# Optimization experiments

Measured on AMD Instinct MI355X. Metric: run time of the kernel, lower is better.

## Reference

```python
import jax, jax.numpy as jnp
import numpy as np

N_NODES = 50000
N_EDGES = 800000
D_IN = 128
D_OUT = 128
NEG_SLOPE = 0.2


def setup_inputs() -> dict:
    key = jax.random.key(0)
    ks = jax.random.split(key, 6)
    stdv = 1.0 / np.sqrt(D_OUT)
    X = jax.random.normal(ks[0], (N_NODES, D_IN), dtype=jnp.float32)
    W = jax.random.uniform(ks[1], (D_IN, D_OUT), dtype=jnp.float32, minval=-stdv, maxval=stdv)
    W_r = jax.random.uniform(ks[2], (D_IN, D_OUT), dtype=jnp.float32, minval=-stdv, maxval=stdv)
    W_l = jax.random.uniform(ks[3], (D_IN, D_OUT), dtype=jnp.float32, minval=-stdv, maxval=stdv)
    src = jax.random.randint(ks[4], (N_EDGES,), 0, N_NODES, dtype=jnp.int32)
    dst = jax.random.randint(ks[5], (N_EDGES,), 0, N_NODES, dtype=jnp.int32)
    return {"X": X, "W": W, "W_r": W_r, "W_l": W_l, "src": src, "dst": dst}


def reference(X, W, W_r, W_l, src, dst):
    # Dense transforms (comb/agg feature paths)
    comb = X @ W            # [N, D_out]
    h_r = X @ W_r           # [N, D_out]
    h_l = X @ W_l           # [N, D_out]
    # SDDMM: per-edge score e_ij = dot(h_l[i], h_r[j]) at nonzeros of A
    e = jnp.sum(h_l[src] * h_r[dst], axis=-1)          # [E]
    e = jax.nn.leaky_relu(e, negative_slope=NEG_SLOPE)  # LeakyReLU(0.2) on edge values
    # SpMM aggregation: agg[i] = sum_{j in N(i)} e_ij * comb[j]
    msgs = e[:, None] * comb[dst]                       # [E, D_out]
    agg = jax.ops.segment_sum(msgs, src, num_segments=N_NODES)  # [N, D_out]
    return agg
```

## Files before the change

kernel.cpp:

```cpp
#include <hip/hip_runtime.h>
#include <hip/hip_bf16.h>

#define N_NODES 50000
#define N_EDGES 800000
#define D 128
#define NEG_SLOPE 0.2f
#define APAD 136

#define FB 196
#define BCAP 8192
#define CHUNK 2048
#define BIN_NBLK ((N_EDGES + CHUNK - 1) / CHUNK)
#define GROWS 64
#define GGRID ((N_NODES + GROWS - 1) / GROWS)
#define GEMM_LDS (D * APAD * 2 + GROWS * APAD * 2)

#define SPMM_NODES 8
#define SPMM_GRID (N_NODES / SPMM_NODES)
#define SPMM_LDS (D * APAD * 2 + 16 * APAD * 2 + 16 * 132 * 4)

typedef __attribute__((ext_vector_type(8))) short bf16x8;
typedef __attribute__((ext_vector_type(4))) float f32x4;

__device__ inline unsigned short f2bf(float f) {
    union { float f; unsigned u; } v; v.f = f;
    const unsigned r = v.u + 0x7FFF + ((v.u >> 16) & 1);
    return (unsigned short)(r >> 16);
}
__device__ inline unsigned fbits(float f) { union { float f; unsigned u; } v; v.f = f; return v.u; }
__device__ inline float ffrom(unsigned u) { union { unsigned u; float f; } v; v.u = u; return v.f; }

__device__ inline void unpack8(const float4 raw, float* o) {
    const unsigned w0 = fbits(raw.x), w1 = fbits(raw.y), w2 = fbits(raw.z), w3 = fbits(raw.w);
    o[0] = ffrom(w0 << 16); o[1] = ffrom(w0 & 0xffff0000u);
    o[2] = ffrom(w1 << 16); o[3] = ffrom(w1 & 0xffff0000u);
    o[4] = ffrom(w2 << 16); o[5] = ffrom(w2 & 0xffff0000u);
    o[6] = ffrom(w3 << 16); o[7] = ffrom(w3 & 0xffff0000u);
}

__device__ __forceinline__ float rsum16(float t) {
    union { float f; int i; } u, s;
    u.f = t;
    s.i = __builtin_amdgcn_update_dpp(0, u.i, 0x128, 0xF, 0xF, true); u.f += s.f;
    s.i = __builtin_amdgcn_update_dpp(0, u.i, 0x124, 0xF, 0xF, true); u.f += s.f;
    s.i = __builtin_amdgcn_update_dpp(0, u.i, 0x4E,  0xF, 0xF, true); u.f += s.f;
    s.i = __builtin_amdgcn_update_dpp(0, u.i, 0x39,  0xF, 0xF, true); u.f += s.f;
    return u.f;
}

__device__ __forceinline__ int scan256_incl_fast(int* wsum, int t, int v) {
    const int lane = t & 63;
    int x = v;
#pragma unroll
    for (int off = 1; off < 64; off <<= 1) {
        const int u = __shfl_up(x, off, 64);
        if (lane >= off) x += u;
    }
    if (lane == 63) wsum[t >> 6] = x;
    __syncthreads();
    int base = 0;
#pragma unroll
    for (int wv = 0; wv < 3; ++wv)
        base += (wv < (t >> 6)) ? wsum[wv] : 0;
    return x + base;
}

__device__ __forceinline__ int scan_incl_512(int* wsum, int t, int v) {
    const int lane = t & 63;
    int x = v;
#pragma unroll
    for (int off = 1; off < 64; off <<= 1) {
        const int u = __shfl_up(x, off, 64);
        if (lane >= off) x += u;
    }
    if (lane == 63) wsum[t >> 6] = x;
    __syncthreads();
    int base = 0;
#pragma unroll
    for (int wv = 0; wv < 7; ++wv)
        base += (wv < (t >> 6)) ? wsum[wv] : 0;
    return x + base;
}

__device__ __forceinline__ void stage_B_lds(unsigned short* Bs, const ushort* __restrict__ BT) {
    const int tid = threadIdx.x;
#pragma unroll
    for (int i = 0; i < 8; ++i) {
        const int idx = tid + i * 256;
        const int row = idx >> 4;
        const int c8 = (idx & 15) << 3;
        const float4 v = ((const float4*)BT)[idx];
        *(float4*)&Bs[row * APAD + c8] = v;
    }
}

template <bool OUT_F32>
__device__ __forceinline__ void mfma_from_lds(const unsigned short* Bs,
                                              const unsigned short* As,
                                              int rb, float* __restrict__ Cf,
                                              ushort* __restrict__ Cb, int nrows) {
    const int tid = threadIdx.x;
    const int w = tid >> 6, lane = tid & 63, m = lane & 15, kq = lane >> 4;
    f32x4 acc[8] = {};
    const unsigned short* Arow = &As[(w * 16 + m) * APAD + kq * 8];
#pragma unroll
    for (int kc = 0; kc < 4; ++kc) {
        const bf16x8 af = *(const bf16x8*)(Arow + kc * 32);
#pragma unroll
        for (int t2 = 0; t2 < 8; ++t2) {
            const bf16x8 bf = *(const bf16x8*)&Bs[(t2 * 16 + m) * APAD + kc * 32 + kq * 8];
            acc[t2] = __builtin_amdgcn_mfma_f32_16x16x32_bf16(af, bf, acc[t2], 0, 0, 0);
        }
    }
    const int orow0 = rb + w * 16 + kq * 4;
#pragma unroll
    for (int t2 = 0; t2 < 8; ++t2) {
#pragma unroll
        for (int r = 0; r < 4; ++r) {
            const int row = orow0 + r;
            if (row < nrows) {
                const size_t o = (size_t)row * D + t2 * 16 + m;
                if (OUT_F32) Cf[o] = acc[t2][r];
                else         Cb[o] = f2bf(acc[t2][r]);
            }
        }
    }
}

__global__ __launch_bounds__(256) void prep_kernel(const float* __restrict__ W_l,
                                                   const float* __restrict__ W_r,
                                                   const float* __restrict__ W,
                                                   ushort* __restrict__ MbT,
                                                   ushort* __restrict__ WbT,
                                                   int* __restrict__ bucket_fill) {
    if (blockIdx.x == 0) bucket_fill[threadIdx.x] = 0;
    const int a = blockIdx.x * 2 + (threadIdx.x >> 7);
    const int b2 = threadIdx.x & 127;
    float acc = 0.f;
#pragma unroll
    for (int c = 0; c < D; c += 4) {
        const float4 wl = *(const float4*)(W_l + a * D + c);
        const float4 wr = *(const float4*)(W_r + b2 * D + c);
        acc += wl.x * wr.x + wl.y * wr.y + wl.z * wr.z + wl.w * wr.w;
    }
    MbT[b2 * D + a] = f2bf(acc);
    WbT[b2 * D + a] = f2bf(W[a * D + b2]);
}

__global__ __launch_bounds__(256) void k1_kernel(const int* __restrict__ src,
                                                 const int* __restrict__ dst,
                                                 int* __restrict__ bucket_fill,
                                                 int2* __restrict__ binned,
                                                 const ushort* __restrict__ MbT,
                                                 const float4* __restrict__ Xf4,
                                                 ushort* __restrict__ Xb,
                                                 ushort* __restrict__ hMb) {
    __shared__ __align__(16) char smem[GEMM_LDS];
    const int bx = blockIdx.x;
    const int t = threadIdx.x;

    if (bx < BIN_NBLK) {
        int*  hist     = (int*)smem;
        int*  bstart   = hist + 256;
        int*  reserveS = bstart + 256;
        int*  fillL    = reserveS + 256;
        int2* pairs    = (int2*)(fillL + 256);
        int*  targ     = (int*)(pairs + CHUNK);
        const int e0 = bx * CHUNK;

        hist[t] = 0;
        __syncthreads();

        int s[8], d[8], b[8];
#pragma unroll
        for (int i = 0; i < 8; ++i) {
            const int e = e0 + i * 256 + t;
            if (e < N_EDGES) {
                s[i] = src[e]; d[i] = dst[e]; b[i] = s[i] >> 8;
                atomicAdd(&hist[b[i]], 1);
            } else b[i] = -1;
        }
        __syncthreads();
        const int hv = hist[t];
        const int incl = scan256_incl_fast(bstart, t, hv);
        const int mystart = incl - hv;
        reserveS[t] = hv ? atomicAdd(&bucket_fill[t], hv) : 0;
        __syncthreads();
        bstart[t] = mystart;
        fillL[t] = mystart;
        __syncthreads();
#pragma unroll
        for (int i = 0; i < 8; ++i) {
            if (b[i] >= 0) {
                const int p = atomicAdd(&fillL[b[i]], 1);
                pairs[p] = make_int2(s[i], d[i]);
                const int pos = reserveS[b[i]] + (p - bstart[b[i]]);
                targ[p] = (pos < BCAP) ? (b[i] * BCAP + pos) : -1;
            }
        }
        __syncthreads();
        const int nval = min(CHUNK, N_EDGES - e0);
        for (int j = t; j < nval; j += 256)
            if (targ[j] >= 0) binned[targ[j]] = pairs[j];
    } else {
        unsigned short* Bs = (unsigned short*)smem;
        unsigned short* As = Bs + D * APAD;
        const int rb = (bx - BIN_NBLK) * GROWS;

        stage_B_lds(Bs, MbT);
#pragma unroll
        for (int i = 0; i < 4; ++i) {
            const int f2 = t + i * 256;
            const int row = f2 >> 4;
            const int c8 = (f2 & 15) << 3;
            ushort4 lo = {0, 0, 0, 0}, hi = {0, 0, 0, 0};
            if (rb + row < N_NODES) {
                const float4 a = Xf4[(size_t)(rb + row) * 32 + (c8 >> 2)];
                const float4 b = Xf4[(size_t)(rb + row) * 32 + (c8 >> 2) + 1];
                lo.x = f2bf(a.x); lo.y = f2bf(a.y); lo.z = f2bf(a.z); lo.w = f2bf(a.w);
                hi.x = f2bf(b.x); hi.y = f2bf(b.y); hi.z = f2bf(b.z); hi.w = f2bf(b.w);
                ushort* gp = Xb + (size_t)(rb + row) * D + c8;
                *(ushort4*)gp = lo;
                *(ushort4*)(gp + 4) = hi;
            }
            *(ushort4*)&As[row * APAD + c8] = lo;
            *(ushort4*)&As[row * APAD + c8 + 4] = hi;
        }
        __syncthreads();
        mfma_from_lds<false>(Bs, As, rb, nullptr, hMb, N_NODES);
    }
}

__global__ __launch_bounds__(512) void fine_kernel(const int2* __restrict__ binned,
                                                   const int* __restrict__ bucket_fill,
                                                   int* __restrict__ offsets,
                                                   int* __restrict__ sorted_dst) {
    __shared__ int cntS[256];
    __shared__ int nh[256];
    __shared__ int fill[256];
    __shared__ int wsum[8];
    __shared__ int dstbuf[BCAP];
    const int b = blockIdx.x;
    const int t = threadIdx.x;

    int cv = 0;
    if (t < 256) cv = (t < FB) ? bucket_fill[t] : 0;
    const int incl = scan_incl_512(wsum, t, cv);
    if (t < 256) cntS[t] = incl;
    __syncthreads();
    const int base = (b == 0) ? 0 : cntS[b - 1];
    int cnt = cntS[b] - base;
    if (cnt > BCAP) cnt = BCAP;

    if (t < 256) nh[t] = 0;
    __syncthreads();
    const int2* bb = binned + (size_t)b * BCAP;
    for (int e = t; e < cnt; e += 512) atomicAdd(&nh[bb[e].x & 255], 1);
    __syncthreads();
    const int v = (t < 256) ? nh[t] : 0;
    const int incl2 = scan_incl_512(wsum, t, v);
    if (t < 256) {
        const int mystart = incl2 - v;
        const int node = b * 256 + t;
        if (node < N_NODES) offsets[node] = base + mystart;
        fill[t] = mystart;
    }
    __syncthreads();
    for (int e = t; e < cnt; e += 512) {
        const int2 sd = bb[e];
        const int p = atomicAdd(&fill[sd.x & 255], 1);
        dstbuf[p] = sd.y;
    }
    __syncthreads();
    for (int j = t; j < cnt; j += 512)
        sorted_dst[base + j] = dstbuf[j];
}

__global__ __launch_bounds__(1024, 8) void spmm_fused_kernel(const ushort* __restrict__ hMb,
                                                             const ushort* __restrict__ Xb,
                                                             const int* __restrict__ offsets,
                                                             const int* __restrict__ sorted_dst,
                                                             const ushort* __restrict__ WbT,
                                                             float* __restrict__ agg) {
    __shared__ __align__(16) char smem[SPMM_LDS];
    unsigned short* Ws = (unsigned short*)smem;
    unsigned short* As = Ws + D * APAD;
    float*          Pf = (float*)(As + 16 * APAD);
    const int tid = threadIdx.x;

#pragma unroll
    for (int i = 0; i < 2; ++i) {
        const int idx = tid + i * 1024;
        const int row = idx >> 4;
        const int c8 = (idx & 15) << 3;
        const float4 v = ((const float4*)WbT)[idx];
        *(float4*)&Ws[row * APAD + c8] = v;
    }
    if (tid < 272) ((ushort4*)(As + 8 * APAD))[tid] = make_ushort4(0, 0, 0, 0);

    const int wave = tid >> 6;
    const int lane = tid & 63;
    const int h = wave & 1;
    const int nl = wave >> 1;
    const int node = blockIdx.x * SPMM_NODES + nl;
    const int q = lane >> 4;
    const int ql = lane & 15;

    float hm[8];
    unpack8(*(const float4*)(hMb + (size_t)node * D + ql * 8), hm);

    const int start = offsets[node];
    const int end = (node == N_NODES - 1) ? N_EDGES : offsets[node + 1];

    float acc[8] = {0.f, 0.f, 0.f, 0.f, 0.f, 0.f, 0.f, 0.f};

    int idx = start + h * 4 + q;
    while (idx + 8 < end) {
        const int d0 = sorted_dst[idx];
        const int d1 = sorted_dst[idx + 8];
        const float4 r0 = *(const float4*)(Xb + (size_t)d0 * D + ql * 8);
        const float4 r1 = *(const float4*)(Xb + (size_t)d1 * D + ql * 8);
        float t0 = 0.f, t1 = 0.f;
        {
            float x[8];
            unpack8(r0, x);
#pragma unroll
            for (int j = 0; j < 8; ++j) t0 = fmaf(hm[j], x[j], t0);
            unpack8(r1, x);
#pragma unroll
            for (int j = 0; j < 8; ++j) t1 = fmaf(hm[j], x[j], t1);
        }
        t0 = rsum16(t0);
        t1 = rsum16(t1);
        const float e0 = t0 > 0.f ? t0 : NEG_SLOPE * t0;
        const float e1 = t1 > 0.f ? t1 : NEG_SLOPE * t1;
        {
            float x[8];
            unpack8(r0, x);
#pragma unroll
            for (int j = 0; j < 8; ++j) acc[j] = fmaf(e0, x[j], acc[j]);
            unpack8(r1, x);
#pragma unroll
            for (int j = 0; j < 8; ++j) acc[j] = fmaf(e1, x[j], acc[j]);
        }
        idx += 16;
    }
    if (idx < end) {
        const int d0 = sorted_dst[idx];
        const float4 r0 = *(const float4*)(Xb + (size_t)d0 * D + ql * 8);
        float t0 = 0.f;
        {
            float x[8];
            unpack8(r0, x);
#pragma unroll
            for (int j = 0; j < 8; ++j) t0 = fmaf(hm[j], x[j], t0);
        }
        t0 = rsum16(t0);
        const float e0 = t0 > 0.f ? t0 : NEG_SLOPE * t0;
        {
            float x[8];
            unpack8(r0, x);
#pragma unroll
            for (int j = 0; j < 8; ++j) acc[j] = fmaf(e0, x[j], acc[j]);
        }
    }

#pragma unroll
    for (int j = 0; j < 8; ++j) {
        acc[j] += __shfl_xor(acc[j], 16);
        acc[j] += __shfl_xor(acc[j], 32);
    }
    if (q == 0) {
        float* p = Pf + (h * 8 + nl) * 132 + ql * 8;
#pragma unroll
        for (int j = 0; j < 8; ++j) p[j] = acc[j];
    }
    __syncthreads();

    if (h == 0 && q == 0) {
        const float* p0 = Pf + nl * 132 + ql * 8;
        const float* p1 = Pf + (8 + nl) * 132 + ql * 8;
        ushort4 o0, o1;
        o0.x = f2bf(p0[0] + p1[0]); o0.y = f2bf(p0[1] + p1[1]);
        o0.z = f2bf(p0[2] + p1[2]); o0.w = f2bf(p0[3] + p1[3]);
        o1.x = f2bf(p0[4] + p1[4]); o1.y = f2bf(p0[5] + p1[5]);
        o1.z = f2bf(p0[6] + p1[6]); o1.w = f2bf(p0[7] + p1[7]);
        *(ushort4*)&As[nl * APAD + ql * 8] = o0;
        *(ushort4*)&As[nl * APAD + ql * 8 + 4] = o1;
    }
    __syncthreads();

    if (wave < 4) {
        const int m = lane & 15, kq = lane >> 4;
        f32x4 oacc[2] = {};
        const unsigned short* Arow = &As[m * APAD + kq * 8];
#pragma unroll
        for (int kc = 0; kc < 4; ++kc) {
            const bf16x8 af = *(const bf16x8*)(Arow + kc * 32);
#pragma unroll
            for (int tt = 0; tt < 2; ++tt) {
                const int t2 = wave * 2 + tt;
                const bf16x8 bf = *(const bf16x8*)&Ws[(t2 * 16 + m) * APAD + kc * 32 + kq * 8];
                oacc[tt] = __builtin_amdgcn_mfma_f32_16x16x32_bf16(af, bf, oacc[tt], 0, 0, 0);
            }
        }
        if (kq < 2) {
            const int rbase = blockIdx.x * SPMM_NODES + kq * 4;
#pragma unroll
            for (int tt = 0; tt < 2; ++tt) {
                const int t2 = wave * 2 + tt;
#pragma unroll
                for (int r = 0; r < 4; ++r) {
                    agg[(size_t)(rbase + r) * D + t2 * 16 + m] = oacc[tt][r];
                }
            }
        }
    }
}

extern "C" void kernel_launch(void* const* d_in, const int* in_sizes, int n_in,
                              void* d_out, int out_size, void* d_ws, size_t ws_size,
                              hipStream_t stream) {
    const float* X   = (const float*)d_in[0];
    const float* W   = (const float*)d_in[1];
    const float* W_r = (const float*)d_in[2];
    const float* W_l = (const float*)d_in[3];
    const int* src   = (const int*)d_in[4];
    const int* dst   = (const int*)d_in[5];
    float* agg = (float*)d_out;

    ushort* Xb          = (ushort*)d_ws;
    ushort* hMb         = Xb + (size_t)N_NODES * D;
    ushort* MbT         = hMb + (size_t)N_NODES * D;
    ushort* WbT         = MbT + D * D;
    int*    offsets     = (int*)(WbT + D * D);
    int*    sorted_dst  = offsets + N_NODES;
    int*    bucket_fill = sorted_dst + N_EDGES;
    int2*   binned      = (int2*)(bucket_fill + 256);

    prep_kernel<<<64, 256, 0, stream>>>(W_l, W_r, W, MbT, WbT, bucket_fill);

    k1_kernel<<<BIN_NBLK + GGRID, 256, 0, stream>>>(
        src, dst, bucket_fill, binned, MbT, (const float4*)X, Xb, hMb);

    fine_kernel<<<FB, 512, 0, stream>>>(binned, bucket_fill, offsets, sorted_dst);

    spmm_fused_kernel<<<SPMM_GRID, 1024, 0, stream>>>(
        hMb, Xb, offsets, sorted_dst, WbT, agg);
}
```

Measured before the change: 167.7 us.

## Assign one wave per node in fused SpMM, fill all MFMA rows, unroll edges by five

The fused SDDMM+SpMM kernel now gives each of 16 waves its own destination node instead of splitting every node across two waves. This removes the float LDS partial buffer and the extra barrier that merged the two halves, and all 16 rows of the MFMA A tile now hold real nodes instead of 8 real rows plus zero padding. The edge loop handles five gathered rows per iteration with clamped indices and zeroed weights past the end, so more loads are in flight and the separate tail loop goes away. In exchange each wave walks a node's full edge list alone, which can lengthen the critical path when degrees vary, and the block count is halved.

```diff
diff --git a/kernel.cpp b/kernel.cpp
--- a/kernel.cpp
+++ b/kernel.cpp
@@ -15,9 +15,9 @@
 #define GGRID ((N_NODES + GROWS - 1) / GROWS)
 #define GEMM_LDS (D * APAD * 2 + GROWS * APAD * 2)
 
-#define SPMM_NODES 8
+#define SPMM_NODES 16
 #define SPMM_GRID (N_NODES / SPMM_NODES)
-#define SPMM_LDS (D * APAD * 2 + 16 * APAD * 2 + 16 * 132 * 4)
+#define SPMM_LDS ((D * APAD + SPMM_NODES * APAD) * 2)
 
 typedef __attribute__((ext_vector_type(8))) short bf16x8;
 typedef __attribute__((ext_vector_type(4))) float f32x4;
@@ -36,6 +36,30 @@
     o[2] = ffrom(w1 << 16); o[3] = ffrom(w1 & 0xffff0000u);
     o[4] = ffrom(w2 << 16); o[5] = ffrom(w2 & 0xffff0000u);
     o[6] = ffrom(w3 << 16); o[7] = ffrom(w3 & 0xffff0000u);
+}
+
+__device__ __forceinline__ float dot8(const float4 r, const float* hm) {
+    const unsigned w0 = fbits(r.x), w1 = fbits(r.y), w2 = fbits(r.z), w3 = fbits(r.w);
+    float t = hm[0] * ffrom(w0 << 16);
+    t = fmaf(hm[1], ffrom(w0 & 0xffff0000u), t);
+    t = fmaf(hm[2], ffrom(w1 << 16), t);
+    t = fmaf(hm[3], ffrom(w1 & 0xffff0000u), t);
+    t = fmaf(hm[4], ffrom(w2 << 16), t);
+    t = fmaf(hm[5], ffrom(w2 & 0xffff0000u), t);
+    t = fmaf(hm[6], ffrom(w3 << 16), t);
+    t = fmaf(hm[7], ffrom(w3 & 0xffff0000u), t);
+    return t;
+}
+__device__ __forceinline__ void accum8(float* acc, float e, const float4 r) {
+    const unsigned w0 = fbits(r.x), w1 = fbits(r.y), w2 = fbits(r.z), w3 = fbits(r.w);
+    acc[0] = fmaf(e, ffrom(w0 << 16), acc[0]);
+    acc[1] = fmaf(e, ffrom(w0 & 0xffff0000u), acc[1]);
+    acc[2] = fmaf(e, ffrom(w1 << 16), acc[2]);
+    acc[3] = fmaf(e, ffrom(w1 & 0xffff0000u), acc[3]);
+    acc[4] = fmaf(e, ffrom(w2 << 16), acc[4]);
+    acc[5] = fmaf(e, ffrom(w2 & 0xffff0000u), acc[5]);
+    acc[6] = fmaf(e, ffrom(w3 << 16), acc[6]);
+    acc[7] = fmaf(e, ffrom(w3 & 0xffff0000u), acc[7]);
 }
 
 __device__ __forceinline__ float rsum16(float t) {
@@ -285,7 +309,6 @@
     __shared__ __align__(16) char smem[SPMM_LDS];
     unsigned short* Ws = (unsigned short*)smem;
     unsigned short* As = Ws + D * APAD;
-    float*          Pf = (float*)(As + 16 * APAD);
     const int tid = threadIdx.x;
 
 #pragma unroll
@@ -296,13 +319,10 @@
         const float4 v = ((const float4*)WbT)[idx];
         *(float4*)&Ws[row * APAD + c8] = v;
     }
-    if (tid < 272) ((ushort4*)(As + 8 * APAD))[tid] = make_ushort4(0, 0, 0, 0);
 
     const int wave = tid >> 6;
     const int lane = tid & 63;
-    const int h = wave & 1;
-    const int nl = wave >> 1;
-    const int node = blockIdx.x * SPMM_NODES + nl;
+    const int node = blockIdx.x * SPMM_NODES + wave;
     const int q = lane >> 4;
     const int ql = lane & 15;
 
@@ -314,55 +334,45 @@
 
     float acc[8] = {0.f, 0.f, 0.f, 0.f, 0.f, 0.f, 0.f, 0.f};
 
-    int idx = start + h * 4 + q;
-    while (idx + 8 < end) {
+    int idx = start + q;
+    while (idx < end) {
+        const int i1 = idx + 4, i2 = idx + 8, i3 = idx + 12, i4 = idx + 16;
         const int d0 = sorted_dst[idx];
-        const int d1 = sorted_dst[idx + 8];
+        const int d1 = sorted_dst[i1 < end ? i1 : idx];
+        const int d2 = sorted_dst[i2 < end ? i2 : idx];
+        const int d3 = sorted_dst[i3 < end ? i3 : idx];
+        const int d4 = sorted_dst[i4 < end ? i4 : idx];
         const float4 r0 = *(const float4*)(Xb + (size_t)d0 * D + ql * 8);
         const float4 r1 = *(const float4*)(Xb + (size_t)d1 * D + ql * 8);
-        float t0 = 0.f, t1 = 0.f;
-        {
-            float x[8];
-            unpack8(r0, x);
-#pragma unroll
-            for (int j = 0; j < 8; ++j) t0 = fmaf(hm[j], x[j], t0);
-            unpack8(r1, x);
-#pragma unroll
-            for (int j = 0; j < 8; ++j) t1 = fmaf(hm[j], x[j], t1);
-        }
+        const float4 r2 = *(const float4*)(Xb + (size_t)d2 * D + ql * 8);
+        const float4 r3 = *(const float4*)(Xb + (size_t)d3 * D + ql * 8);
+        const float4 r4 = *(const float4*)(Xb + (size_t)d4 * D + ql * 8);
+
+        float t0 = dot8(r0, hm);
+        float t1 = dot8(r1, hm);
+        float t2 = dot8(r2, hm);
+        float t3 = dot8(r3, hm);
+        float t4 = dot8(r4, hm);
         t0 = rsum16(t0);
         t1 = rsum16(t1);
+        t2 = rsum16(t2);
+        t3 = rsum16(t3);
+        t4 = rsum16(t4);
         const float e0 = t0 > 0.f ? t0 : NEG_SLOPE * t0;
-        const float e1 = t1 > 0.f ? t1 : NEG_SLOPE * t1;
-        {
-            float x[8];
-            unpack8(r0, x);
-#pragma unroll
-            for (int j = 0; j < 8; ++j) acc[j] = fmaf(e0, x[j], acc[j]);
-            unpack8(r1, x);
-#pragma unroll
-            for (int j = 0; j < 8; ++j) acc[j] = fmaf(e1, x[j], acc[j]);
-        }
-        idx += 16;
-    }
-    if (idx < end) {
-        const int d0 = sorted_dst[idx];
-        const float4 r0 = *(const float4*)(Xb + (size_t)d0 * D + ql * 8);
-        float t0 = 0.f;
-        {
-            float x[8];
-            unpack8(r0, x);
-#pragma unroll
-            for (int j = 0; j < 8; ++j) t0 = fmaf(hm[j], x[j], t0);
-        }
-        t0 = rsum16(t0);
-        const float e0 = t0 > 0.f ? t0 : NEG_SLOPE * t0;
-        {
-            float x[8];
-            unpack8(r0, x);
-#pragma unroll
-            for (int j = 0; j < 8; ++j) acc[j] = fmaf(e0, x[j], acc[j]);
-        }
+        float e1 = t1 > 0.f ? t1 : NEG_SLOPE * t1;
+        float e2 = t2 > 0.f ? t2 : NEG_SLOPE * t2;
+        float e3 = t3 > 0.f ? t3 : NEG_SLOPE * t3;
+        float e4 = t4 > 0.f ? t4 : NEG_SLOPE * t4;
+        e1 = (i1 < end) ? e1 : 0.f;
+        e2 = (i2 < end) ? e2 : 0.f;
+        e3 = (i3 < end) ? e3 : 0.f;
+        e4 = (i4 < end) ? e4 : 0.f;
+        accum8(acc, e0, r0);
+        accum8(acc, e1, r1);
+        accum8(acc, e2, r2);
+        accum8(acc, e3, r3);
+        accum8(acc, e4, r4);
+        idx += 20;
     }
 
 #pragma unroll
@@ -371,22 +381,11 @@
         acc[j] += __shfl_xor(acc[j], 32);
     }
     if (q == 0) {
-        float* p = Pf + (h * 8 + nl) * 132 + ql * 8;
-#pragma unroll
-        for (int j = 0; j < 8; ++j) p[j] = acc[j];
-    }
-    __syncthreads();
-
-    if (h == 0 && q == 0) {
-        const float* p0 = Pf + nl * 132 + ql * 8;
-        const float* p1 = Pf + (8 + nl) * 132 + ql * 8;
         ushort4 o0, o1;
-        o0.x = f2bf(p0[0] + p1[0]); o0.y = f2bf(p0[1] + p1[1]);
-        o0.z = f2bf(p0[2] + p1[2]); o0.w = f2bf(p0[3] + p1[3]);
-        o1.x = f2bf(p0[4] + p1[4]); o1.y = f2bf(p0[5] + p1[5]);
-        o1.z = f2bf(p0[6] + p1[6]); o1.w = f2bf(p0[7] + p1[7]);
-        *(ushort4*)&As[nl * APAD + ql * 8] = o0;
-        *(ushort4*)&As[nl * APAD + ql * 8 + 4] = o1;
+        o0.x = f2bf(acc[0]); o0.y = f2bf(acc[1]); o0.z = f2bf(acc[2]); o0.w = f2bf(acc[3]);
+        o1.x = f2bf(acc[4]); o1.y = f2bf(acc[5]); o1.z = f2bf(acc[6]); o1.w = f2bf(acc[7]);
+        *(ushort4*)&As[wave * APAD + ql * 8] = o0;
+        *(ushort4*)&As[wave * APAD + ql * 8 + 4] = o1;
     }
     __syncthreads();
 
@@ -404,15 +403,13 @@
                 oacc[tt] = __builtin_amdgcn_mfma_f32_16x16x32_bf16(af, bf, oacc[tt], 0, 0, 0);
             }
         }
-        if (kq < 2) {
-            const int rbase = blockIdx.x * SPMM_NODES + kq * 4;
-#pragma unroll
-            for (int tt = 0; tt < 2; ++tt) {
-                const int t2 = wave * 2 + tt;
-#pragma unroll
-                for (int r = 0; r < 4; ++r) {
-                    agg[(size_t)(rbase + r) * D + t2 * 16 + m] = oacc[tt][r];
-                }
+        const int rbase = blockIdx.x * SPMM_NODES + kq * 4;
+#pragma unroll
+        for (int tt = 0; tt < 2; ++tt) {
+            const int t2 = wave * 2 + tt;
+#pragma unroll
+            for (int r = 0; r < 4; ++r) {
+                agg[(size_t)(rbase + r) * D + t2 * 16 + m] = oacc[tt][r];
             }
         }
     }
```

Result: slower. 278.5 us (+66.1%).
